# Kernel tuning notes

Measured on AMD Instinct MI355X. Metric: run time of the kernel, lower is better.

## Reference

```python
import jax, jax.numpy as jnp
import numpy as np


def _unfold(x, k, pad, stride):
    # torch F.unfold: [B,C,H,W] -> [B, C*k*k, L] with (C, kh, kw) channel-major ordering
    B, C, H, W = x.shape
    xp = jnp.pad(x, ((0, 0), (0, 0), (pad, pad), (pad, pad)))
    oh = (H + 2 * pad - k) // stride + 1
    ow = (W + 2 * pad - k) // stride + 1
    rows = (jnp.arange(oh) * stride)[:, None] + jnp.arange(k)[None, :]  # [oh,k]
    cols = (jnp.arange(ow) * stride)[:, None] + jnp.arange(k)[None, :]  # [ow,k]
    p = xp[:, :, rows][:, :, :, :, cols]          # [B,C,oh,k,ow,k]
    p = p.transpose(0, 1, 3, 5, 2, 4)             # [B,C,k,k,oh,ow]
    return p.reshape(B, C * k * k, oh * ow)


def _fold(p, out_hw, k, pad, stride):
    # torch F.fold: overlap-add of patches [B, C*k*k, L] -> [B,C,H,W]
    B = p.shape[0]
    C = p.shape[1] // (k * k)
    H, W = out_hw
    oh = (H + 2 * pad - k) // stride + 1
    ow = (W + 2 * pad - k) // stride + 1
    p = p.reshape(B, C, k, k, oh, ow).transpose(0, 1, 4, 2, 5, 3)  # [B,C,oh,k,ow,k]
    rows = (jnp.arange(oh) * stride)[:, None] + jnp.arange(k)[None, :]  # [oh,k]
    cols = (jnp.arange(ow) * stride)[:, None] + jnp.arange(k)[None, :]  # [ow,k]
    out = jnp.zeros((B, C, H + 2 * pad, W + 2 * pad), p.dtype)
    out = out.at[:, :, rows[:, :, None, None], cols[None, None, :, :]].add(p)
    return out[:, :, pad:pad + H, pad:pad + W]


def _bis_gather(unf, idx):
    # torch.gather along dim=2 with per-batch index broadcast over channels
    return jnp.take_along_axis(unf, idx[:, None, :], axis=2)


def setup_inputs() -> dict:
    key = jax.random.key(0)
    k1, k2, k3, k4 = jax.random.split(key, 4)
    B, H, W = 4, 96, 96
    L = H * W
    return {
        "R_lv2_star_arg": jax.random.randint(k1, (B, L), 0, L, dtype=jnp.int64 if jax.config.jax_enable_x64 else jnp.int32).astype(jnp.int32),
        "lrsr_lv2": jax.random.normal(k2, (B, 64, H, W), dtype=jnp.float32),
        "ref_lv1": jax.random.normal(k3, (B, 64, 2 * H, 2 * W), dtype=jnp.float32),
        "ref_lv2": jax.random.normal(k4, (B, 128, H, W), dtype=jnp.float32),
    }


def reference(R_lv2_star_arg, lrsr_lv2, ref_lv1, ref_lv2):
    H, W = lrsr_lv2.shape[2], lrsr_lv2.shape[3]
    ref_lv2_unfold = _unfold(ref_lv2, 3, 1, 1)   # [B, C2*9, H*W]
    ref_lv1_unfold = _unfold(ref_lv1, 6, 2, 2)   # [B, C1*36, H*W]
    T_lv2_unfold = _bis_gather(ref_lv2_unfold, R_lv2_star_arg)
    T_lv1_unfold = _bis_gather(ref_lv1_unfold, R_lv2_star_arg)
    T_lv2 = _fold(T_lv2_unfold, (H, W), 3, 1, 1) / 9.0
    T_lv1 = _fold(T_lv1_unfold, (2 * H, 2 * W), 6, 2, 2) / 9.0
    return (T_lv2, T_lv1)
```

## Files before the change

### kernel.cpp

```cpp
#include <hip/hip_runtime.h>


typedef float f2 __attribute__((ext_vector_type(2)));
typedef float f4 __attribute__((ext_vector_type(4)));

#define NINE_INV (1.0f / 9.0f)
#define ZOFF 73728u

__device__ __forceinline__ unsigned rne_bf16(float f) {
    unsigned u = __builtin_bit_cast(unsigned, f);
    return (u + 0x7fffu + ((u >> 16) & 1u)) >> 16;
}
__device__ __forceinline__ unsigned pack_bf2(float a, float b) {
    return rne_bf16(a) | (rne_bf16(b) << 16);
}
__device__ __forceinline__ f2 up2(unsigned w) {
    f2 r;
    r.x = __builtin_bit_cast(float, w << 16);
    r.y = __builtin_bit_cast(float, w & 0xffff0000u);
    return r;
}

__global__ __launch_bounds__(256) void table_kernel(
    const int* __restrict__ idx, unsigned* __restrict__ tab)
{
    int g = blockIdx.x * 256 + threadIdx.x;
    int b = g >> 13 >= 0 ? g / 9216 : 0;
    int u = g - b * 9216;
    const int* idxb = idx + b * 9216;
    unsigned* tb = tab + (size_t)b * 9 * 9216;
    int r = u / 96, t = u - 96 * r;
#pragma unroll
    for (int i = 0; i < 3; ++i) {
        int oy = r - 1 + i;
        bool oyv = (unsigned)oy < 96u;
#pragma unroll
        for (int j = 0; j < 3; ++j) {
            int ox = t - 1 + j;
            bool pv = oyv & ((unsigned)ox < 96u);
            int jv = idxb[pv ? oy * 96 + ox : 0];
            int jy = jv / 96, jx = jv - 96 * jy;
            int ysh = jy + 1 - i, xsh = jx + 1 - j;
            bool sv = pv & ((unsigned)ysh < 96u) & ((unsigned)xsh < 96u);
            tb[(i * 3 + j) * 9216 + u] = sv ? (unsigned)((ysh * 96 + xsh) * 8) : ZOFF;
        }
    }
}

template <bool TAB>
__global__ __launch_bounds__(512) void transfer_kernel(
    const int* __restrict__ idx,
    const float* __restrict__ ref1,
    const float* __restrict__ ref2,
    const unsigned* __restrict__ tab,
    float* __restrict__ out)
{
    __shared__ __align__(16) unsigned s2[18436];
    const int tid = threadIdx.x;
    const int bid = blockIdx.x;
    const int b = bid & 3;

    if (tid < 4) s2[18432 + tid] = 0;

    const unsigned* tb = tab + (size_t)b * 9 * 9216;
    const int* idxb = idx + b * 9216;

    if (bid < 256) {
        const int q = (bid >> 2) & 1, c0 = (bid >> 3) * 2;
        const float* g0 = ref1 + (size_t)(b * 64 + c0) * 36864;

        for (int u2 = tid; u2 < 4608; u2 += 512) {
            int ysh = u2 / 48, xsh0 = 2 * (u2 - 48 * ysh);
            const float* gp = g0 + (size_t)(2 * ysh + q) * 192 + 2 * xsh0;
            f4 va = *(const f4*)gp;
            f4 vb = *(const f4*)(gp + 36864);
            uint4 w;
            w.x = pack_bf2(va.x, va.y); w.y = pack_bf2(vb.x, vb.y);
            w.z = pack_bf2(va.z, va.w); w.w = pack_bf2(vb.z, vb.w);
            *(uint4*)(s2 + 4 * u2) = w;
        }
        __syncthreads();

        float* ob = out + 4718592 + (size_t)(b * 64 + c0) * 36864;

        for (int u = tid; u < 9216; u += 512) {
            unsigned o[9];
            if (TAB) {
#pragma unroll
                for (int p = 0; p < 9; ++p) o[p] = tb[p * 9216 + u];
            } else {
                int r = u / 96, t = u - 96 * r;
#pragma unroll
                for (int i = 0; i < 3; ++i) {
                    int oy = r - 1 + i;
                    bool oyv = (unsigned)oy < 96u;
#pragma unroll
                    for (int j = 0; j < 3; ++j) {
                        int ox = t - 1 + j;
                        bool pv = oyv & ((unsigned)ox < 96u);
                        int jv = idxb[pv ? oy * 96 + ox : 0];
                        int jy = jv / 96, jx = jv - 96 * jy;
                        int ysh = jy + 1 - i, xsh = jx + 1 - j;
                        bool sv = pv & ((unsigned)ysh < 96u) & ((unsigned)xsh < 96u);
                        o[i * 3 + j] = sv ? (unsigned)((ysh * 96 + xsh) * 8) : ZOFF;
                    }
                }
            }
            f2 a0 = {0.f, 0.f}, a1 = {0.f, 0.f};
#pragma unroll
            for (int p = 0; p < 9; ++p) {
                uint2 w = *(const uint2*)((const char*)s2 + o[p]);
                a0 += up2(w.x);
                a1 += up2(w.y);
            }
            f2 nv = {NINE_INV, NINE_INV};
            a0 *= nv; a1 *= nv;
            int r = u / 96, t = u - 96 * r;
            int y = 2 * r + q, x0 = 2 * t;
            float* op = ob + (size_t)y * 192 + x0;
            *(f2*)op = a0;
            *(f2*)(op + 36864) = a1;
        }
    } else {
        const int r2 = bid - 256;
        const int grp = (r2 >> 2) & 31, h = (r2 >> 7) & 1;
        const int c0 = grp * 4;
        const float* g0 = ref2 + (size_t)(b * 128 + c0) * 9216;

        for (int u2 = tid; u2 < 4608; u2 += 512) {
            f2 p0 = *(const f2*)(g0 + 2 * u2);
            f2 p1 = *(const f2*)(g0 + 9216 + 2 * u2);
            f2 p2 = *(const f2*)(g0 + 2 * 9216 + 2 * u2);
            f2 p3 = *(const f2*)(g0 + 3 * 9216 + 2 * u2);
            uint4 w;
            w.x = pack_bf2(p0.x, p1.x); w.y = pack_bf2(p2.x, p3.x);
            w.z = pack_bf2(p0.y, p1.y); w.w = pack_bf2(p2.y, p3.y);
            *(uint4*)(s2 + 4 * u2) = w;
        }
        __syncthreads();

        float* ob = out + (size_t)(b * 128 + c0) * 9216;

        const int u0 = h * 4608, u1 = u0 + 4608;
        for (int u = u0 + tid; u < u1; u += 512) {
            unsigned o[9];
            if (TAB) {
#pragma unroll
                for (int p = 0; p < 9; ++p) o[p] = tb[p * 9216 + u];
            } else {
                int y = u / 96, x = u - 96 * y;
#pragma unroll
                for (int i = 0; i < 3; ++i) {
                    int oy = y - 1 + i;
                    bool oyv = (unsigned)oy < 96u;
#pragma unroll
                    for (int j = 0; j < 3; ++j) {
                        int ox = x - 1 + j;
                        bool pv = oyv & ((unsigned)ox < 96u);
                        int jv = idxb[pv ? oy * 96 + ox : 0];
                        int jy = jv / 96, jx = jv - 96 * jy;
                        int ys = jy + 1 - i, xs = jx + 1 - j;
                        bool sv = pv & ((unsigned)ys < 96u) & ((unsigned)xs < 96u);
                        o[i * 3 + j] = sv ? (unsigned)((ys * 96 + xs) * 8) : ZOFF;
                    }
                }
            }
            f2 a0 = {0.f, 0.f}, a1 = {0.f, 0.f};
#pragma unroll
            for (int p = 0; p < 9; ++p) {
                uint2 w = *(const uint2*)((const char*)s2 + o[p]);
                a0 += up2(w.x);
                a1 += up2(w.y);
            }
            f2 nv = {NINE_INV, NINE_INV};
            a0 *= nv; a1 *= nv;
            float* op = ob + u;
            op[0]        = a0.x; op[9216]     = a0.y;
            op[2 * 9216] = a1.x; op[3 * 9216] = a1.y;
        }
    }
}

extern "C" void kernel_launch(void* const* d_in, const int* in_sizes, int n_in,
                              void* d_out, int out_size, void* d_ws, size_t ws_size,
                              hipStream_t stream) {
    const int*   idx  = (const int*)d_in[0];
    const float* ref1 = (const float*)d_in[2];
    const float* ref2 = (const float*)d_in[3];
    float* outp = (float*)d_out;
    unsigned* tab = (unsigned*)d_ws;

    const size_t need = (size_t)4 * 9 * 9216 * sizeof(unsigned);
    if (ws_size >= need) {
        hipLaunchKernelGGL(table_kernel, dim3(144), dim3(256), 0, stream, idx, tab);
        hipLaunchKernelGGL(transfer_kernel<true>, dim3(512), dim3(512), 0, stream,
                           idx, ref1, ref2, tab, outp);
    } else {
        hipLaunchKernelGGL(transfer_kernel<false>, dim3(512), dim3(512), 0, stream,
                           idx, ref1, ref2, tab, outp);
    }
}
```

Baseline: 31.28 us.

## Pack offset table to 16-bit cells, prefetch table rows, use nontemporal loads/stores

The per-pixel tap offset table is stored as nine 16-bit cell indices (one uint4 plus one ushort) instead of nine 32-bit byte offsets. This cuts table traffic roughly in half, and each thread fetches it with one vector load. The transfer loops now prefetch the next iteration's table entry, and input staging loads and output stores use nontemporal hints. Launch bounds add a minimum-occupancy hint. Register pressure from prefetching and the occupancy hint may trade against these gains.

```diff
diff --git a/kernel.cpp b/kernel.cpp
--- a/kernel.cpp
+++ b/kernel.cpp
@@ -5,7 +5,7 @@
 typedef float f4 __attribute__((ext_vector_type(4)));
 
 #define NINE_INV (1.0f / 9.0f)
-#define ZOFF 73728u
+#define ZCELL 9216u
 
 __device__ __forceinline__ unsigned rne_bf16(float f) {
     unsigned u = __builtin_bit_cast(unsigned, f);
@@ -20,16 +20,23 @@
     r.y = __builtin_bit_cast(float, w & 0xffff0000u);
     return r;
 }
+template <typename T> __device__ __forceinline__ T ntload(const T* p) {
+    return __builtin_nontemporal_load(p);
+}
+template <typename T> __device__ __forceinline__ void ntstore(T* p, T v) {
+    __builtin_nontemporal_store(v, p);
+}
 
 __global__ __launch_bounds__(256) void table_kernel(
-    const int* __restrict__ idx, unsigned* __restrict__ tab)
+    const int* __restrict__ idx, uint4* __restrict__ tabA,
+    unsigned short* __restrict__ tabB)
 {
     int g = blockIdx.x * 256 + threadIdx.x;
-    int b = g >> 13 >= 0 ? g / 9216 : 0;
+    int b = g / 9216;
     int u = g - b * 9216;
     const int* idxb = idx + b * 9216;
-    unsigned* tb = tab + (size_t)b * 9 * 9216;
     int r = u / 96, t = u - 96 * r;
+    unsigned e[9];
 #pragma unroll
     for (int i = 0; i < 3; ++i) {
         int oy = r - 1 + i;
@@ -42,17 +49,25 @@
             int jy = jv / 96, jx = jv - 96 * jy;
             int ysh = jy + 1 - i, xsh = jx + 1 - j;
             bool sv = pv & ((unsigned)ysh < 96u) & ((unsigned)xsh < 96u);
-            tb[(i * 3 + j) * 9216 + u] = sv ? (unsigned)((ysh * 96 + xsh) * 8) : ZOFF;
+            e[i * 3 + j] = sv ? (unsigned)(ysh * 96 + xsh) : ZCELL;
         }
     }
+    uint4 w;
+    w.x = e[0] | (e[1] << 16);
+    w.y = e[2] | (e[3] << 16);
+    w.z = e[4] | (e[5] << 16);
+    w.w = e[6] | (e[7] << 16);
+    tabA[g] = w;
+    tabB[g] = (unsigned short)e[8];
 }
 
 template <bool TAB>
-__global__ __launch_bounds__(512) void transfer_kernel(
+__global__ __launch_bounds__(512, 4) void transfer_kernel(
     const int* __restrict__ idx,
     const float* __restrict__ ref1,
     const float* __restrict__ ref2,
-    const unsigned* __restrict__ tab,
+    const uint4* __restrict__ tabA,
+    const unsigned short* __restrict__ tabB,
     float* __restrict__ out)
 {
     __shared__ __align__(16) unsigned s2[18436];
@@ -62,8 +77,41 @@
 
     if (tid < 4) s2[18432 + tid] = 0;
 
-    const unsigned* tb = tab + (size_t)b * 9 * 9216;
+    const uint4* tA = tabA + b * 9216;
+    const unsigned short* tB = tabB + b * 9216;
     const int* idxb = idx + b * 9216;
+
+    auto inline_cells = [&](int u, unsigned* e) {
+        int r = u / 96, t = u - 96 * r;
+#pragma unroll
+        for (int i = 0; i < 3; ++i) {
+            int oy = r - 1 + i;
+            bool oyv = (unsigned)oy < 96u;
+#pragma unroll
+            for (int j = 0; j < 3; ++j) {
+                int ox = t - 1 + j;
+                bool pv = oyv & ((unsigned)ox < 96u);
+                int jv = idxb[pv ? oy * 96 + ox : 0];
+                int jy = jv / 96, jx = jv - 96 * jy;
+                int ysh = jy + 1 - i, xsh = jx + 1 - j;
+                bool sv = pv & ((unsigned)ysh < 96u) & ((unsigned)xsh < 96u);
+                e[i * 3 + j] = sv ? (unsigned)(ysh * 96 + xsh) : ZCELL;
+            }
+        }
+    };
+
+    auto do_taps = [&](const unsigned* cw, unsigned c8, f2& a0, f2& a1) {
+#pragma unroll
+        for (int q = 0; q < 4; ++q) {
+            unsigned lo = cw[q] & 0xffffu, hi = cw[q] >> 16;
+            uint2 wa = *(const uint2*)((const char*)s2 + (lo << 3));
+            uint2 wb = *(const uint2*)((const char*)s2 + (hi << 3));
+            a0 += up2(wa.x); a1 += up2(wa.y);
+            a0 += up2(wb.x); a1 += up2(wb.y);
+        }
+        uint2 wc = *(const uint2*)((const char*)s2 + (c8 << 3));
+        a0 += up2(wc.x); a1 += up2(wc.y);
+    };
 
     if (bid < 256) {
         const int q = (bid >> 2) & 1, c0 = (bid >> 3) * 2;
@@ -72,8 +120,8 @@
         for (int u2 = tid; u2 < 4608; u2 += 512) {
             int ysh = u2 / 48, xsh0 = 2 * (u2 - 48 * ysh);
             const float* gp = g0 + (size_t)(2 * ysh + q) * 192 + 2 * xsh0;
-            f4 va = *(const f4*)gp;
-            f4 vb = *(const f4*)(gp + 36864);
+            f4 va = ntload((const f4*)gp);
+            f4 vb = ntload((const f4*)(gp + 36864));
             uint4 w;
             w.x = pack_bf2(va.x, va.y); w.y = pack_bf2(vb.x, vb.y);
             w.z = pack_bf2(va.z, va.w); w.w = pack_bf2(vb.z, vb.w);
@@ -83,43 +131,33 @@
 
         float* ob = out + 4718592 + (size_t)(b * 64 + c0) * 36864;
 
-        for (int u = tid; u < 9216; u += 512) {
-            unsigned o[9];
+        uint4 cA; unsigned cB;
+        if (TAB) { cA = tA[tid]; cB = tB[tid]; }
+        int u = tid;
+#pragma unroll 2
+        for (int k = 0; k < 18; ++k) {
+            uint4 nA = cA; unsigned nB = cB;
+            if (TAB && k < 17) { nA = tA[u + 512]; nB = tB[u + 512]; }
+            unsigned cw[4];
+            unsigned c8;
             if (TAB) {
-#pragma unroll
-                for (int p = 0; p < 9; ++p) o[p] = tb[p * 9216 + u];
+                cw[0] = cA.x; cw[1] = cA.y; cw[2] = cA.z; cw[3] = cA.w; c8 = cB;
             } else {
-                int r = u / 96, t = u - 96 * r;
-#pragma unroll
-                for (int i = 0; i < 3; ++i) {
-                    int oy = r - 1 + i;
-                    bool oyv = (unsigned)oy < 96u;
-#pragma unroll
-                    for (int j = 0; j < 3; ++j) {
-                        int ox = t - 1 + j;
-                        bool pv = oyv & ((unsigned)ox < 96u);
-                        int jv = idxb[pv ? oy * 96 + ox : 0];
-                        int jy = jv / 96, jx = jv - 96 * jy;
-                        int ysh = jy + 1 - i, xsh = jx + 1 - j;
-                        bool sv = pv & ((unsigned)ysh < 96u) & ((unsigned)xsh < 96u);
-                        o[i * 3 + j] = sv ? (unsigned)((ysh * 96 + xsh) * 8) : ZOFF;
-                    }
-                }
+                unsigned e[9];
+                inline_cells(u, e);
+                cw[0] = e[0] | (e[1] << 16); cw[1] = e[2] | (e[3] << 16);
+                cw[2] = e[4] | (e[5] << 16); cw[3] = e[6] | (e[7] << 16);
+                c8 = e[8];
             }
             f2 a0 = {0.f, 0.f}, a1 = {0.f, 0.f};
-#pragma unroll
-            for (int p = 0; p < 9; ++p) {
-                uint2 w = *(const uint2*)((const char*)s2 + o[p]);
-                a0 += up2(w.x);
-                a1 += up2(w.y);
-            }
+            do_taps(cw, c8, a0, a1);
             f2 nv = {NINE_INV, NINE_INV};
             a0 *= nv; a1 *= nv;
             int r = u / 96, t = u - 96 * r;
-            int y = 2 * r + q, x0 = 2 * t;
-            float* op = ob + (size_t)y * 192 + x0;
-            *(f2*)op = a0;
-            *(f2*)(op + 36864) = a1;
+            float* op = ob + (size_t)(2 * r + q) * 192 + 2 * t;
+            ntstore((f2*)op, a0);
+            ntstore((f2*)(op + 36864), a1);
+            u += 512; cA = nA; cB = nB;
         }
     } else {
         const int r2 = bid - 256;
@@ -128,10 +166,10 @@
         const float* g0 = ref2 + (size_t)(b * 128 + c0) * 9216;
 
         for (int u2 = tid; u2 < 4608; u2 += 512) {
-            f2 p0 = *(const f2*)(g0 + 2 * u2);
-            f2 p1 = *(const f2*)(g0 + 9216 + 2 * u2);
-            f2 p2 = *(const f2*)(g0 + 2 * 9216 + 2 * u2);
-            f2 p3 = *(const f2*)(g0 + 3 * 9216 + 2 * u2);
+            f2 p0 = ntload((const f2*)(g0 + 2 * u2));
+            f2 p1 = ntload((const f2*)(g0 + 9216 + 2 * u2));
+            f2 p2 = ntload((const f2*)(g0 + 2 * 9216 + 2 * u2));
+            f2 p3 = ntload((const f2*)(g0 + 3 * 9216 + 2 * u2));
             uint4 w;
             w.x = pack_bf2(p0.x, p1.x); w.y = pack_bf2(p2.x, p3.x);
             w.z = pack_bf2(p0.y, p1.y); w.w = pack_bf2(p2.y, p3.y);
@@ -141,42 +179,33 @@
 
         float* ob = out + (size_t)(b * 128 + c0) * 9216;
 
-        const int u0 = h * 4608, u1 = u0 + 4608;
-        for (int u = u0 + tid; u < u1; u += 512) {
-            unsigned o[9];
+        const int u0 = h * 4608;
+        uint4 cA; unsigned cB;
+        if (TAB) { cA = tA[u0 + tid]; cB = tB[u0 + tid]; }
+        int u = u0 + tid;
+#pragma unroll 2
+        for (int k = 0; k < 9; ++k) {
+            uint4 nA = cA; unsigned nB = cB;
+            if (TAB && k < 8) { nA = tA[u + 512]; nB = tB[u + 512]; }
+            unsigned cw[4];
+            unsigned c8;
             if (TAB) {
-#pragma unroll
-                for (int p = 0; p < 9; ++p) o[p] = tb[p * 9216 + u];
+                cw[0] = cA.x; cw[1] = cA.y; cw[2] = cA.z; cw[3] = cA.w; c8 = cB;
             } else {
-                int y = u / 96, x = u - 96 * y;
-#pragma unroll
-                for (int i = 0; i < 3; ++i) {
-                    int oy = y - 1 + i;
-                    bool oyv = (unsigned)oy < 96u;
-#pragma unroll
-                    for (int j = 0; j < 3; ++j) {
-                        int ox = x - 1 + j;
-                        bool pv = oyv & ((unsigned)ox < 96u);
-                        int jv = idxb[pv ? oy * 96 + ox : 0];
-                        int jy = jv / 96, jx = jv - 96 * jy;
-                        int ys = jy + 1 - i, xs = jx + 1 - j;
-                        bool sv = pv & ((unsigned)ys < 96u) & ((unsigned)xs < 96u);
-                        o[i * 3 + j] = sv ? (unsigned)((ys * 96 + xs) * 8) : ZOFF;
-                    }
-                }
+                unsigned e[9];
+                inline_cells(u, e);
+                cw[0] = e[0] | (e[1] << 16); cw[1] = e[2] | (e[3] << 16);
+                cw[2] = e[4] | (e[5] << 16); cw[3] = e[6] | (e[7] << 16);
+                c8 = e[8];
             }
             f2 a0 = {0.f, 0.f}, a1 = {0.f, 0.f};
-#pragma unroll
-            for (int p = 0; p < 9; ++p) {
-                uint2 w = *(const uint2*)((const char*)s2 + o[p]);
-                a0 += up2(w.x);
-                a1 += up2(w.y);
-            }
+            do_taps(cw, c8, a0, a1);
             f2 nv = {NINE_INV, NINE_INV};
             a0 *= nv; a1 *= nv;
             float* op = ob + u;
-            op[0]        = a0.x; op[9216]     = a0.y;
-            op[2 * 9216] = a1.x; op[3 * 9216] = a1.y;
+            ntstore(op, a0.x);          ntstore(op + 9216, a0.y);
+            ntstore(op + 2 * 9216, a1.x); ntstore(op + 3 * 9216, a1.y);
+            u += 512; cA = nA; cB = nB;
         }
     }
 }
@@ -188,15 +217,18 @@
     const float* ref1 = (const float*)d_in[2];
     const float* ref2 = (const float*)d_in[3];
     float* outp = (float*)d_out;
-    unsigned* tab = (unsigned*)d_ws;
-
-    const size_t need = (size_t)4 * 9 * 9216 * sizeof(unsigned);
+
+    uint4* tabA = (uint4*)d_ws;
+    unsigned short* tabB = (unsigned short*)((char*)d_ws + (size_t)4 * 9216 * 16);
+
+    const size_t need = (size_t)4 * 9216 * 16 + (size_t)4 * 9216 * 2;
     if (ws_size >= need) {
-        hipLaunchKernelGGL(table_kernel, dim3(144), dim3(256), 0, stream, idx, tab);
+        hipLaunchKernelGGL(table_kernel, dim3(144), dim3(256), 0, stream,
+                           idx, tabA, tabB);
         hipLaunchKernelGGL(transfer_kernel<true>, dim3(512), dim3(512), 0, stream,
-                           idx, ref1, ref2, tab, outp);
+                           idx, ref1, ref2, tabA, tabB, outp);
     } else {
         hipLaunchKernelGGL(transfer_kernel<false>, dim3(512), dim3(512), 0, stream,
-                           idx, ref1, ref2, tab, outp);
+                           idx, ref1, ref2, tabA, tabB, outp);
     }
 }
```

Measured after the change: 28.06 us. 10.3% less time.
